# Kernel tuning notes

Measured on AMD Instinct MI355X. Metric: run time of the kernel, lower is better.

Reference implementation:

```python
import jax, jax.numpy as jnp
import numpy as np
from functools import partial

HID = 256
HOR = 5

def _lin(k, i, o):
    return jax.random.normal(k, (i, o), jnp.float32) / np.sqrt(i)

def setup_inputs() -> dict:
    key = jax.random.key(0)
    ks = jax.random.split(key, 32)
    B, T, D, Hf, Wf = 4, 16, 768, 16, 16
    H, W = 1024, 1024
    inp = {}
    inp['features'] = jax.random.normal(ks[0], (B, T, D, Hf, Wf), jnp.float32)
    inp['predictions'] = jax.random.uniform(ks[1], (B, T, 1, H, W), dtype=jnp.float32)
    # position encoder: 4 -> HID -> HID
    inp['pe_w1'] = _lin(ks[2], 4, HID); inp['pe_b1'] = jnp.zeros((HID,), jnp.float32)
    inp['pe_w2'] = _lin(ks[3], HID, HID); inp['pe_b2'] = jnp.zeros((HID,), jnp.float32)
    # 2-layer LSTM, gate order i,f,g,o (torch convention)
    inp['wih0'] = _lin(ks[4], HID, 4 * HID); inp['whh0'] = _lin(ks[5], HID, 4 * HID)
    inp['bih0'] = jnp.zeros((4 * HID,), jnp.float32); inp['bhh0'] = jnp.zeros((4 * HID,), jnp.float32)
    inp['wih1'] = _lin(ks[6], HID, 4 * HID); inp['whh1'] = _lin(ks[7], HID, 4 * HID)
    inp['bih1'] = jnp.zeros((4 * HID,), jnp.float32); inp['bhh1'] = jnp.zeros((4 * HID,), jnp.float32)
    # motion predictor: HID -> HID -> HID/2 -> HOR*4
    inp['mp_w1'] = _lin(ks[8], HID, HID); inp['mp_b1'] = jnp.zeros((HID,), jnp.float32)
    inp['mp_w2'] = _lin(ks[9], HID, HID // 2); inp['mp_b2'] = jnp.zeros((HID // 2,), jnp.float32)
    inp['mp_w3'] = _lin(ks[10], HID // 2, HOR * 4); inp['mp_b3'] = jnp.zeros((HOR * 4,), jnp.float32)
    # confidence: HID -> HID/2 -> HOR
    inp['cf_w1'] = _lin(ks[11], HID, HID // 2); inp['cf_b1'] = jnp.zeros((HID // 2,), jnp.float32)
    inp['cf_w2'] = _lin(ks[12], HID // 2, HOR); inp['cf_b2'] = jnp.zeros((HOR,), jnp.float32)
    return inp

def _extract_bboxes(predictions):
    # predictions: (B,T,1,H,W) -> bboxes (B,T,4) in (cx,cy,w,h), normalized
    B, T, _, H, W = predictions.shape
    mask = predictions[:, :, 0] > 0.5  # (B,T,H,W)
    xs = jnp.arange(W, dtype=jnp.float32)           # (W,)
    ys = jnp.arange(H, dtype=jnp.float32)[:, None]  # (H,1)
    big = jnp.float32(H + W)
    x_min = jnp.min(jnp.where(mask, xs, big), axis=(-2, -1))
    x_max = jnp.max(jnp.where(mask, xs, -1.0), axis=(-2, -1))
    y_min = jnp.min(jnp.where(mask, ys, big), axis=(-2, -1))
    y_max = jnp.max(jnp.where(mask, ys, -1.0), axis=(-2, -1))
    has = jnp.any(mask, axis=(-2, -1))  # (B,T)
    cx = (x_min + x_max) / 2.0 / W
    cy = (y_min + y_max) / 2.0 / H
    w = (x_max - x_min) / W
    h = (y_max - y_min) / H
    bbox = jnp.stack([cx, cy, w, h], axis=-1)  # (B,T,4)
    default = jnp.array([0.5, 0.5, 0.1, 0.1], dtype=jnp.float32)
    return jnp.where(has[..., None], bbox, default)

def _lstm_layer(x, wih, whh, bih, bhh):
    # x: (B,T,HID); returns (hs (B,T,H), h_final (B,H))
    B = x.shape[0]
    xg = jnp.einsum('bti,ig->btg', x, wih) + bih  # (B,T,4H)
    def step(carry, xg_t):
        h, c = carry
        g = xg_t + h @ whh + bhh
        i, f, gg, o = jnp.split(g, 4, axis=-1)
        i = jax.nn.sigmoid(i); f = jax.nn.sigmoid(f)
        gg = jnp.tanh(gg); o = jax.nn.sigmoid(o)
        c = f * c + i * gg
        h = o * jnp.tanh(c)
        return (h, c), h
    z = jnp.zeros((B, HID), x.dtype)
    (h, c), hs = jax.lax.scan(step, (z, z), xg.swapaxes(0, 1))
    return hs.swapaxes(0, 1), h

def reference(features, predictions, pe_w1, pe_b1, pe_w2, pe_b2,
              wih0, whh0, bih0, bhh0, wih1, whh1, bih1, bhh1,
              mp_w1, mp_b1, mp_w2, mp_b2, mp_w3, mp_b3,
              cf_w1, cf_b1, cf_w2, cf_b2):
    B, T = features.shape[:2]
    bboxes = _extract_bboxes(predictions)  # (B,T,4)
    pos = jax.nn.relu(bboxes @ pe_w1 + pe_b1)
    pos = jax.nn.relu(pos @ pe_w2 + pe_b2)  # (B,T,HID)
    h1, _ = _lstm_layer(pos, wih0, whh0, bih0, bhh0)
    motion_features, last_hidden = _lstm_layer(h1, wih1, whh1, bih1, bhh1)
    x = jax.nn.relu(last_hidden @ mp_w1 + mp_b1)
    x = jax.nn.relu(x @ mp_w2 + mp_b2)
    predicted_deltas = (x @ mp_w3 + mp_b3).reshape(B, HOR, 4)
    last_bbox = bboxes[:, -1:, :]
    predicted_bboxes = last_bbox + jnp.cumsum(predicted_deltas, axis=1)
    c = jax.nn.relu(last_hidden @ cf_w1 + cf_b1)
    confidence = jax.nn.sigmoid(c @ cf_w2 + cf_b2)  # (B,HOR)
    predicted_locations = predicted_bboxes[..., :2]
    predicted_scales = predicted_bboxes[..., 2:]
    return (predicted_deltas, predicted_bboxes, predicted_locations,
            predicted_scales, motion_features, confidence, bboxes)
```

## Files before the change

### kernel.cpp

```cpp
#include <hip/hip_runtime.h>
#include <math.h>

#define BIGI (1 << 30)

#define PM_OFF    0
#define HT0_OFF   8192
#define HT2_OFF   40960
#define DONE_OFF  45056
#define ZERO_BEG  8192
#define ZERO_END  45057

#define OUT_DELTAS 0
#define OUT_PBB    80
#define OUT_LOC    160
#define OUT_SCL    200
#define OUT_MF     240
#define OUT_CONF   16624
#define OUT_BBOX   16644

__device__ __forceinline__ float sigmoidf_(float x) { return 1.0f / (1.0f + expf(-x)); }

__device__ __forceinline__ void storeh(unsigned long long* p, float h, int tag) {
    unsigned long long v =
        ((unsigned long long)(unsigned)tag << 32) | (unsigned long long)__float_as_uint(h);
    __hip_atomic_store(p, v, __ATOMIC_RELAXED, __HIP_MEMORY_SCOPE_AGENT);
}
__device__ __forceinline__ float pollh(const unsigned long long* p, int tag) {
    unsigned long long v = __hip_atomic_load(p, __ATOMIC_RELAXED, __HIP_MEMORY_SCOPE_AGENT);
    while ((int)(v >> 32) != tag) {
        __builtin_amdgcn_s_sleep(1);
        v = __hip_atomic_load(p, __ATOMIC_RELAXED, __HIP_MEMORY_SCOPE_AGENT);
    }
    return __uint_as_float((unsigned)v);
}

__global__ __launch_bounds__(256) void k_minmax(const float4* __restrict__ pred,
                                                int* __restrict__ ws) {
    int tid = threadIdx.x;
    for (int i = ZERO_BEG + blockIdx.x * 256 + tid; i < ZERO_END; i += 2048 * 256)
        ws[i] = 0;
    int img = blockIdx.x >> 5;
    int chunk = blockIdx.x & 31;
    int base = img * 262144 + chunk * 8192 + tid;
    int xmn = BIGI, xmx = -1, ymn = BIGI, ymx = -1;
#pragma unroll 4
    for (int i = 0; i < 32; ++i) {
        int idx4 = base + i * 256;
        float4 v = pred[idx4];
        int x = (idx4 << 2) & 1023;
        int y = (idx4 >> 8) & 1023;
        bool m0 = v.x > 0.5f, m1 = v.y > 0.5f, m2 = v.z > 0.5f, m3 = v.w > 0.5f;
        int cmn = m0 ? x : (m1 ? x + 1 : (m2 ? x + 2 : (m3 ? x + 3 : BIGI)));
        int cmx = m3 ? x + 3 : (m2 ? x + 2 : (m1 ? x + 1 : (m0 ? x : -1)));
        xmn = min(xmn, cmn);
        xmx = max(xmx, cmx);
        if (m0 | m1 | m2 | m3) { ymn = min(ymn, y); ymx = max(ymx, y); }
    }
    for (int off = 32; off > 0; off >>= 1) {
        xmn = min(xmn, __shfl_down(xmn, off));
        xmx = max(xmx, __shfl_down(xmx, off));
        ymn = min(ymn, __shfl_down(ymn, off));
        ymx = max(ymx, __shfl_down(ymx, off));
    }
    __shared__ int red[4][4];
    int wave = tid >> 6;
    if ((tid & 63) == 0) { red[0][wave] = xmn; red[1][wave] = xmx; red[2][wave] = ymn; red[3][wave] = ymx; }
    __syncthreads();
    if (tid == 0) {
        xmn = min(min(red[0][0], red[0][1]), min(red[0][2], red[0][3]));
        xmx = max(max(red[1][0], red[1][1]), max(red[1][2], red[1][3]));
        ymn = min(min(red[2][0], red[2][1]), min(red[2][2], red[2][3]));
        ymx = max(max(red[3][0], red[3][1]), max(red[3][2], red[3][3]));
        ((int4*)(ws + PM_OFF))[blockIdx.x] = make_int4(xmn, xmx, ymn, ymx);
    }
}

__device__ __forceinline__ void mk_bbox(int xmn, int xmx, int ymn, int ymx,
                                        float* o) {
    if (xmx >= 0) {
        o[0] = (float)(xmn + xmx) * (0.5f / 1024.0f);
        o[1] = (float)(ymn + ymx) * (0.5f / 1024.0f);
        o[2] = (float)(xmx - xmn) * (1.0f / 1024.0f);
        o[3] = (float)(ymx - ymn) * (1.0f / 1024.0f);
    } else { o[0] = 0.5f; o[1] = 0.5f; o[2] = 0.1f; o[3] = 0.1f; }
}

__global__ __launch_bounds__(256, 1) void k_fused(
    const float* __restrict__ pe_w1, const float* __restrict__ pe_b1,
    const float* __restrict__ pe_w2, const float* __restrict__ pe_b2,
    const float* __restrict__ wih0, const float* __restrict__ whh0,
    const float* __restrict__ bih0, const float* __restrict__ bhh0,
    const float* __restrict__ wih1, const float* __restrict__ whh1,
    const float* __restrict__ bih1, const float* __restrict__ bhh1,
    const float* __restrict__ mp_w1, const float* __restrict__ mp_b1,
    const float* __restrict__ mp_w2, const float* __restrict__ mp_b2,
    const float* __restrict__ mp_w3, const float* __restrict__ mp_b3,
    const float* __restrict__ cf_w1, const float* __restrict__ cf_b1,
    const float* __restrict__ cf_w2, const float* __restrict__ cf_b2,
    const int4* __restrict__ pm4, unsigned long long* __restrict__ hT0,
    unsigned long long* __restrict__ hT2, int* __restrict__ done,
    float* __restrict__ out) {
    __shared__ float sPX[4096];
    __shared__ float sP1[4096];
    __shared__ float sBB[64];
    __shared__ float hsm[256];
    __shared__ float h2sm[256];
    __shared__ float part[256];
    const int tid = threadIdx.x, blk = blockIdx.x;

    if (blk >= 64) {
        float a0 = 0.f, a1 = 1.f, a2 = 2.f, a3 = 3.f, a4 = 4.f, a5 = 5.f, a6 = 6.f, a7 = 7.f;
        const float m = 1.0000001f, c = 0.9999999f;
        for (;;) {
#pragma unroll
            for (int i = 0; i < 128; ++i) {
                a0 = fmaf(a0, m, c); a1 = fmaf(a1, m, c); a2 = fmaf(a2, m, c); a3 = fmaf(a3, m, c);
                a4 = fmaf(a4, m, c); a5 = fmaf(a5, m, c); a6 = fmaf(a6, m, c); a7 = fmaf(a7, m, c);
            }
            if (__hip_atomic_load(done, __ATOMIC_RELAXED, __HIP_MEMORY_SCOPE_AGENT) >= 4) break;
        }
        asm volatile("" :: "v"(a0), "v"(a1), "v"(a2), "v"(a3), "v"(a4), "v"(a5), "v"(a6), "v"(a7));
        return;
    }

    const int layer = blk >> 5;
    const int b = (blk >> 3) & 3, g = blk & 7;
    const int j = tid & 127, kh = tid >> 7;
    const int col = ((j >> 5) << 8) + g * 32 + (j & 31);

    if (layer == 0) {
        {
            int il = tid >> 4, c2 = (tid & 15) * 2;
            int4 A = pm4[(b * 16 + il) * 32 + c2];
            int4 B = pm4[(b * 16 + il) * 32 + c2 + 1];
            int xmn = min(A.x, B.x), xmx = max(A.y, B.y);
            int ymn = min(A.z, B.z), ymx = max(A.w, B.w);
            for (int off = 8; off > 0; off >>= 1) {
                xmn = min(xmn, __shfl_down(xmn, off, 16));
                xmx = max(xmx, __shfl_down(xmx, off, 16));
                ymn = min(ymn, __shfl_down(ymn, off, 16));
                ymx = max(ymx, __shfl_down(ymx, off, 16));
            }
            if ((tid & 15) == 0) {
                float bb[4];
                mk_bbox(xmn, xmx, ymn, ymx, bb);
                sBB[il * 4 + 0] = bb[0]; sBB[il * 4 + 1] = bb[1];
                sBB[il * 4 + 2] = bb[2]; sBB[il * 4 + 3] = bb[3];
                if (g == 0) {
                    out[OUT_BBOX + (b * 16 + il) * 4 + 0] = bb[0];
                    out[OUT_BBOX + (b * 16 + il) * 4 + 1] = bb[1];
                    out[OUT_BBOX + (b * 16 + il) * 4 + 2] = bb[2];
                    out[OUT_BBOX + (b * 16 + il) * 4 + 3] = bb[3];
                }
            }
        }
        __syncthreads();
        {
            float w0 = pe_w1[tid], w1 = pe_w1[256 + tid];
            float w2 = pe_w1[512 + tid], w3 = pe_w1[768 + tid], b1v = pe_b1[tid];
#pragma unroll
            for (int i = 0; i < 16; ++i) {
                float v = sBB[i * 4] * w0 + sBB[i * 4 + 1] * w1 +
                          sBB[i * 4 + 2] * w2 + sBB[i * 4 + 3] * w3 + b1v;
                sP1[i * 256 + tid] = fmaxf(v, 0.0f);
            }
        }
        __syncthreads();
        {
            float acc[16];
            float b2v = pe_b2[tid];
#pragma unroll
            for (int i = 0; i < 16; ++i) acc[i] = b2v;
            for (int k = 0; k < 256; ++k) {
                float wv = pe_w2[k * 256 + tid];
#pragma unroll
                for (int i = 0; i < 16; ++i) acc[i] += sP1[i * 256 + k] * wv;
            }
#pragma unroll
            for (int i = 0; i < 16; ++i) sPX[i * 256 + tid] = fmaxf(acc[i], 0.0f);
        }
        __syncthreads();
    }

    const float* wih = layer ? wih1 : wih0;
    const float* whh = layer ? whh1 : whh0;
    const float* bih = layer ? bih1 : bih0;
    const float* bhh = layer ? bhh1 : bhh0;
    float4 wi[32], wh[32];
#pragma unroll
    for (int k4 = 0; k4 < 32; ++k4) {
        int r = kh * 128 + k4 * 4;
        wi[k4].x = wih[(r + 0) * 1024 + col];
        wi[k4].y = wih[(r + 1) * 1024 + col];
        wi[k4].z = wih[(r + 2) * 1024 + col];
        wi[k4].w = wih[(r + 3) * 1024 + col];
        wh[k4].x = whh[(r + 0) * 1024 + col];
        wh[k4].y = whh[(r + 1) * 1024 + col];
        wh[k4].z = whh[(r + 2) * 1024 + col];
        wh[k4].w = whh[(r + 3) * 1024 + col];
    }
    float bs0 = 0.f, bs1 = 0.f, bs2 = 0.f, bs3 = 0.f;
    if (tid < 32) {
        int u = g * 32 + tid;
        bs0 = bih[u] + bhh[u];
        bs1 = bih[256 + u] + bhh[256 + u];
        bs2 = bih[512 + u] + bhh[512 + u];
        bs3 = bih[768 + u] + bhh[768 + u];
    }

    float cst = 0.0f;
    for (int t = 0; t < 16; ++t) {
        if (layer == 0) {
            if (t) hsm[tid] = pollh(&hT0[((b * 16 + t - 1) << 8) + tid], t);
        } else {
            hsm[tid] = pollh(&hT0[((b * 16 + t) << 8) + tid], t + 1);
            if (t) h2sm[tid] = pollh(&hT2[(((b << 1) | ((t - 1) & 1)) << 8) + tid], t);
        }
        __syncthreads();
        float a = 0.0f;
        if (layer == 0) {
            const float4* xr = (const float4*)&sPX[t * 256 + kh * 128];
#pragma unroll
            for (int k = 0; k < 32; ++k) {
                float4 x = xr[k];
                a += x.x * wi[k].x + x.y * wi[k].y + x.z * wi[k].z + x.w * wi[k].w;
            }
            if (t) {
                const float4* hr = (const float4*)&hsm[kh * 128];
#pragma unroll
                for (int k = 0; k < 32; ++k) {
                    float4 h = hr[k];
                    a += h.x * wh[k].x + h.y * wh[k].y + h.z * wh[k].z + h.w * wh[k].w;
                }
            }
        } else {
            const float4* xr = (const float4*)&hsm[kh * 128];
#pragma unroll
            for (int k = 0; k < 32; ++k) {
                float4 x = xr[k];
                a += x.x * wi[k].x + x.y * wi[k].y + x.z * wi[k].z + x.w * wi[k].w;
            }
            if (t) {
                const float4* hr = (const float4*)&h2sm[kh * 128];
#pragma unroll
                for (int k = 0; k < 32; ++k) {
                    float4 h = hr[k];
                    a += h.x * wh[k].x + h.y * wh[k].y + h.z * wh[k].z + h.w * wh[k].w;
                }
            }
        }
        part[tid] = a;
        __syncthreads();
        if (tid < 32) {
            float gi = part[tid] + part[128 + tid] + bs0;
            float gf = part[32 + tid] + part[160 + tid] + bs1;
            float gg = part[64 + tid] + part[192 + tid] + bs2;
            float go = part[96 + tid] + part[224 + tid] + bs3;
            float i_ = sigmoidf_(gi), f_ = sigmoidf_(gf);
            float g_ = tanhf(gg), o_ = sigmoidf_(go);
            cst = f_ * cst + i_ * g_;
            float h = o_ * tanhf(cst);
            int unit = g * 32 + tid;
            if (layer == 0) {
                storeh(&hT0[((b * 16 + t) << 8) + unit], h, t + 1);
            } else {
                storeh(&hT2[(((b << 1) | (t & 1)) << 8) + unit], h, t + 1);
                out[OUT_MF + (b * 16 + t) * 256 + unit] = h;
            }
        }
    }
    if (layer == 0 || g != 0) return;

    float* lh = sPX;
    float* x1 = sPX + 256;
    float* c1 = sPX + 512;
    float* x2 = sPX + 640;
    float* dl = sPX + 768;
    lh[tid] = pollh(&hT2[(((b << 1) | 1) << 8) + tid], 16);
    if (tid < 32) {
        int4 v = pm4[(b * 16 + 15) * 32 + tid];
        int xmn = v.x, xmx = v.y, ymn = v.z, ymx = v.w;
        for (int off = 16; off > 0; off >>= 1) {
            xmn = min(xmn, __shfl_down(xmn, off, 32));
            xmx = max(xmx, __shfl_down(xmx, off, 32));
            ymn = min(ymn, __shfl_down(ymn, off, 32));
            ymx = max(ymx, __shfl_down(ymx, off, 32));
        }
        if (tid == 0) mk_bbox(xmn, xmx, ymn, ymx, sBB);
    }
    __syncthreads();
    {
        float a = mp_b1[tid];
#pragma unroll 4
        for (int k = 0; k < 256; ++k) a += lh[k] * mp_w1[k * 256 + tid];
        x1[tid] = fmaxf(a, 0.0f);
    }
    if (tid < 128) {
        float a = cf_b1[tid];
#pragma unroll 4
        for (int k = 0; k < 256; ++k) a += lh[k] * cf_w1[k * 128 + tid];
        c1[tid] = fmaxf(a, 0.0f);
    }
    __syncthreads();
    if (tid < 128) {
        float a = mp_b2[tid];
#pragma unroll 4
        for (int k = 0; k < 256; ++k) a += x1[k] * mp_w2[k * 128 + tid];
        x2[tid] = fmaxf(a, 0.0f);
    } else if (tid < 133) {
        int jj = tid - 128;
        float a = cf_b2[jj];
#pragma unroll 4
        for (int k = 0; k < 128; ++k) a += c1[k] * cf_w2[k * 5 + jj];
        out[OUT_CONF + b * 5 + jj] = sigmoidf_(a);
    }
    __syncthreads();
    if (tid < 20) {
        float a = mp_b3[tid];
#pragma unroll 4
        for (int k = 0; k < 128; ++k) a += x2[k] * mp_w3[k * 20 + tid];
        dl[tid] = a;
        out[OUT_DELTAS + b * 20 + tid] = a;
    }
    __syncthreads();
    if (tid < 4) {
        float acc = sBB[tid];
        for (int hh = 0; hh < 5; ++hh) {
            acc += dl[hh * 4 + tid];
            out[OUT_PBB + b * 20 + hh * 4 + tid] = acc;
            if (tid < 2) out[OUT_LOC + b * 10 + hh * 2 + tid] = acc;
            else out[OUT_SCL + b * 10 + hh * 2 + (tid - 2)] = acc;
        }
    }
    __syncthreads();
    if (tid == 0) atomicAdd(done, 1);
}

extern "C" void kernel_launch(void* const* d_in, const int* in_sizes, int n_in,
                              void* d_out, int out_size, void* d_ws, size_t ws_size,
                              hipStream_t stream) {
    (void)in_sizes; (void)n_in; (void)out_size; (void)ws_size;
    const float* pred = (const float*)d_in[1];
    const float* pe_w1 = (const float*)d_in[2];
    const float* pe_b1 = (const float*)d_in[3];
    const float* pe_w2 = (const float*)d_in[4];
    const float* pe_b2 = (const float*)d_in[5];
    const float* wih0 = (const float*)d_in[6];
    const float* whh0 = (const float*)d_in[7];
    const float* bih0 = (const float*)d_in[8];
    const float* bhh0 = (const float*)d_in[9];
    const float* wih1 = (const float*)d_in[10];
    const float* whh1 = (const float*)d_in[11];
    const float* bih1 = (const float*)d_in[12];
    const float* bhh1 = (const float*)d_in[13];
    const float* mp_w1 = (const float*)d_in[14];
    const float* mp_b1 = (const float*)d_in[15];
    const float* mp_w2 = (const float*)d_in[16];
    const float* mp_b2 = (const float*)d_in[17];
    const float* mp_w3 = (const float*)d_in[18];
    const float* mp_b3 = (const float*)d_in[19];
    const float* cf_w1 = (const float*)d_in[20];
    const float* cf_b1 = (const float*)d_in[21];
    const float* cf_w2 = (const float*)d_in[22];
    const float* cf_b2 = (const float*)d_in[23];
    float* out = (float*)d_out;
    int* wsi = (int*)d_ws;

    hipLaunchKernelGGL(k_minmax, dim3(64 * 32), dim3(256), 0, stream,
                       (const float4*)pred, wsi);
    hipLaunchKernelGGL(k_fused, dim3(192), dim3(256), 0, stream,
                       pe_w1, pe_b1, pe_w2, pe_b2,
                       wih0, whh0, bih0, bhh0,
                       wih1, whh1, bih1, bhh1,
                       mp_w1, mp_b1, mp_w2, mp_b2, mp_w3, mp_b3,
                       cf_w1, cf_b1, cf_w2, cf_b2,
                       (const int4*)(wsi + PM_OFF),
                       (unsigned long long*)(wsi + HT0_OFF),
                       (unsigned long long*)(wsi + HT2_OFF),
                       wsi + DONE_OFF, out);
}
```

Before: 603.6 us.

## Split LSTM recurrence across 16 unit groups and precompute layer-0 input gates

Doubles the per-batch LSTM workers from 8 to 16 blocks per layer (16 units each, 4-way K split), so each thread keeps half as many weight registers. Layer 0 precomputes its input-projection gates for all timesteps before the recurrence, so the serial loop only does the hidden-state matvec. Layer 1 polls both dependency slots in one combined helper, and the spinning filler blocks are adjusted for the new grid of 256. The cost is a wider cross-block polling fan-in per step and extra shared memory.

```diff
diff --git a/kernel.cpp b/kernel.cpp
--- a/kernel.cpp
+++ b/kernel.cpp
@@ -32,6 +32,20 @@
         v = __hip_atomic_load(p, __ATOMIC_RELAXED, __HIP_MEMORY_SCOPE_AGENT);
     }
     return __uint_as_float((unsigned)v);
+}
+__device__ __forceinline__ float2 pollh2(const unsigned long long* p1, int tag1,
+                                         const unsigned long long* p2, int tag2) {
+    unsigned long long v1 = __hip_atomic_load(p1, __ATOMIC_RELAXED, __HIP_MEMORY_SCOPE_AGENT);
+    unsigned long long v2 = __hip_atomic_load(p2, __ATOMIC_RELAXED, __HIP_MEMORY_SCOPE_AGENT);
+    while ((int)(v1 >> 32) != tag1) {
+        __builtin_amdgcn_s_sleep(1);
+        v1 = __hip_atomic_load(p1, __ATOMIC_RELAXED, __HIP_MEMORY_SCOPE_AGENT);
+    }
+    while ((int)(v2 >> 32) != tag2) {
+        __builtin_amdgcn_s_sleep(1);
+        v2 = __hip_atomic_load(p2, __ATOMIC_RELAXED, __HIP_MEMORY_SCOPE_AGENT);
+    }
+    return make_float2(__uint_as_float((unsigned)v1), __uint_as_float((unsigned)v2));
 }
 
 __global__ __launch_bounds__(256) void k_minmax(const float4* __restrict__ pred,
@@ -75,8 +89,7 @@
     }
 }
 
-__device__ __forceinline__ void mk_bbox(int xmn, int xmx, int ymn, int ymx,
-                                        float* o) {
+__device__ __forceinline__ void mk_bbox(int xmn, int xmx, int ymn, int ymx, float* o) {
     if (xmx >= 0) {
         o[0] = (float)(xmn + xmx) * (0.5f / 1024.0f);
         o[1] = (float)(ymn + ymx) * (0.5f / 1024.0f);
@@ -100,20 +113,21 @@
     const int4* __restrict__ pm4, unsigned long long* __restrict__ hT0,
     unsigned long long* __restrict__ hT2, int* __restrict__ done,
     float* __restrict__ out) {
-    __shared__ float sPX[4096];
-    __shared__ float sP1[4096];
+    __shared__ __align__(16) float sPX[4096];
+    __shared__ __align__(16) float sP1[4096];
+    __shared__ float xgl[1024];
+    __shared__ __align__(16) float hsm[256];
+    __shared__ __align__(16) float h2sm[256];
+    __shared__ float partA[256];
     __shared__ float sBB[64];
-    __shared__ float hsm[256];
-    __shared__ float h2sm[256];
-    __shared__ float part[256];
     const int tid = threadIdx.x, blk = blockIdx.x;
 
-    if (blk >= 64) {
+    if (blk >= 128) {
         float a0 = 0.f, a1 = 1.f, a2 = 2.f, a3 = 3.f, a4 = 4.f, a5 = 5.f, a6 = 6.f, a7 = 7.f;
         const float m = 1.0000001f, c = 0.9999999f;
         for (;;) {
-#pragma unroll
-            for (int i = 0; i < 128; ++i) {
+#pragma unroll 8
+            for (int i = 0; i < 512; ++i) {
                 a0 = fmaf(a0, m, c); a1 = fmaf(a1, m, c); a2 = fmaf(a2, m, c); a3 = fmaf(a3, m, c);
                 a4 = fmaf(a4, m, c); a5 = fmaf(a5, m, c); a6 = fmaf(a6, m, c); a7 = fmaf(a7, m, c);
             }
@@ -123,10 +137,27 @@
         return;
     }
 
-    const int layer = blk >> 5;
-    const int b = (blk >> 3) & 3, g = blk & 7;
-    const int j = tid & 127, kh = tid >> 7;
-    const int col = ((j >> 5) << 8) + g * 32 + (j & 31);
+    const int layer = blk >> 6;
+    const int b = (blk >> 4) & 3, g = blk & 15;
+    const int cidx = tid & 63, kq = tid >> 6;
+    const int gate = cidx >> 4, u = cidx & 15;
+    const int col = gate * 256 + g * 16 + u;
+    const int krow0 = kq * 64;
+
+    const float* wih = layer ? wih1 : wih0;
+    const float* whh = layer ? whh1 : whh0;
+    const float* bih = layer ? bih1 : bih0;
+    const float* bhh = layer ? bhh1 : bhh0;
+
+    float4 wvi[16];
+#pragma unroll
+    for (int k4 = 0; k4 < 16; ++k4) {
+        int r = krow0 + k4 * 4;
+        wvi[k4].x = wih[(r + 0) * 1024 + col];
+        wvi[k4].y = wih[(r + 1) * 1024 + col];
+        wvi[k4].z = wih[(r + 2) * 1024 + col];
+        wvi[k4].w = wih[(r + 3) * 1024 + col];
+    }
 
     if (layer == 0) {
         {
@@ -180,32 +211,44 @@
             for (int i = 0; i < 16; ++i) sPX[i * 256 + tid] = fmaxf(acc[i], 0.0f);
         }
         __syncthreads();
-    }
-
-    const float* wih = layer ? wih1 : wih0;
-    const float* whh = layer ? whh1 : whh0;
-    const float* bih = layer ? bih1 : bih0;
-    const float* bhh = layer ? bhh1 : bhh0;
-    float4 wi[32], wh[32];
-#pragma unroll
-    for (int k4 = 0; k4 < 32; ++k4) {
-        int r = kh * 128 + k4 * 4;
-        wi[k4].x = wih[(r + 0) * 1024 + col];
-        wi[k4].y = wih[(r + 1) * 1024 + col];
-        wi[k4].z = wih[(r + 2) * 1024 + col];
-        wi[k4].w = wih[(r + 3) * 1024 + col];
-        wh[k4].x = whh[(r + 0) * 1024 + col];
-        wh[k4].y = whh[(r + 1) * 1024 + col];
-        wh[k4].z = whh[(r + 2) * 1024 + col];
-        wh[k4].w = whh[(r + 3) * 1024 + col];
+        float bsum = 0.0f;
+        if (tid < 64) {
+            int cc = (tid >> 4) * 256 + g * 16 + (tid & 15);
+            bsum = bih[cc] + bhh[cc];
+        }
+        for (int t = 0; t < 16; ++t) {
+            const float4* xr = (const float4*)&sPX[t * 256 + krow0];
+            float a = 0.0f;
+#pragma unroll
+            for (int k = 0; k < 16; ++k) {
+                float4 x = xr[k];
+                a += x.x * wvi[k].x + x.y * wvi[k].y + x.z * wvi[k].z + x.w * wvi[k].w;
+            }
+            partA[tid] = a;
+            __syncthreads();
+            if (tid < 64)
+                xgl[t * 64 + tid] = partA[tid] + partA[64 + tid] +
+                                    partA[128 + tid] + partA[192 + tid] + bsum;
+            __syncthreads();
+        }
+    }
+
+    float4 wvh[16];
+#pragma unroll
+    for (int k4 = 0; k4 < 16; ++k4) {
+        int r = krow0 + k4 * 4;
+        wvh[k4].x = whh[(r + 0) * 1024 + col];
+        wvh[k4].y = whh[(r + 1) * 1024 + col];
+        wvh[k4].z = whh[(r + 2) * 1024 + col];
+        wvh[k4].w = whh[(r + 3) * 1024 + col];
     }
     float bs0 = 0.f, bs1 = 0.f, bs2 = 0.f, bs3 = 0.f;
-    if (tid < 32) {
-        int u = g * 32 + tid;
-        bs0 = bih[u] + bhh[u];
-        bs1 = bih[256 + u] + bhh[256 + u];
-        bs2 = bih[512 + u] + bhh[512 + u];
-        bs3 = bih[768 + u] + bhh[768 + u];
+    if (layer == 1 && tid < 16) {
+        int uu = g * 16 + tid;
+        bs0 = bih[uu] + bhh[uu];
+        bs1 = bih[256 + uu] + bhh[256 + uu];
+        bs2 = bih[512 + uu] + bhh[512 + uu];
+        bs3 = bih[768 + uu] + bhh[768 + uu];
     }
 
     float cst = 0.0f;
@@ -213,54 +256,61 @@
         if (layer == 0) {
             if (t) hsm[tid] = pollh(&hT0[((b * 16 + t - 1) << 8) + tid], t);
         } else {
-            hsm[tid] = pollh(&hT0[((b * 16 + t) << 8) + tid], t + 1);
-            if (t) h2sm[tid] = pollh(&hT2[(((b << 1) | ((t - 1) & 1)) << 8) + tid], t);
+            if (t) {
+                float2 hv = pollh2(&hT0[((b * 16 + t) << 8) + tid], t + 1,
+                                   &hT2[(((b << 1) | ((t - 1) & 1)) << 8) + tid], t);
+                hsm[tid] = hv.x; h2sm[tid] = hv.y;
+            } else {
+                hsm[tid] = pollh(&hT0[((b * 16) << 8) + tid], 1);
+            }
         }
         __syncthreads();
         float a = 0.0f;
         if (layer == 0) {
-            const float4* xr = (const float4*)&sPX[t * 256 + kh * 128];
-#pragma unroll
-            for (int k = 0; k < 32; ++k) {
+            if (t) {
+                const float4* hr = (const float4*)&hsm[krow0];
+#pragma unroll
+                for (int k = 0; k < 16; ++k) {
+                    float4 h = hr[k];
+                    a += h.x * wvh[k].x + h.y * wvh[k].y + h.z * wvh[k].z + h.w * wvh[k].w;
+                }
+            }
+        } else {
+            const float4* xr = (const float4*)&hsm[krow0];
+#pragma unroll
+            for (int k = 0; k < 16; ++k) {
                 float4 x = xr[k];
-                a += x.x * wi[k].x + x.y * wi[k].y + x.z * wi[k].z + x.w * wi[k].w;
+                a += x.x * wvi[k].x + x.y * wvi[k].y + x.z * wvi[k].z + x.w * wvi[k].w;
             }
             if (t) {
-                const float4* hr = (const float4*)&hsm[kh * 128];
-#pragma unroll
-                for (int k = 0; k < 32; ++k) {
+                const float4* hr = (const float4*)&h2sm[krow0];
+#pragma unroll
+                for (int k = 0; k < 16; ++k) {
                     float4 h = hr[k];
-                    a += h.x * wh[k].x + h.y * wh[k].y + h.z * wh[k].z + h.w * wh[k].w;
+                    a += h.x * wvh[k].x + h.y * wvh[k].y + h.z * wvh[k].z + h.w * wvh[k].w;
                 }
             }
-        } else {
-            const float4* xr = (const float4*)&hsm[kh * 128];
-#pragma unroll
-            for (int k = 0; k < 32; ++k) {
-                float4 x = xr[k];
-                a += x.x * wi[k].x + x.y * wi[k].y + x.z * wi[k].z + x.w * wi[k].w;
-            }
-            if (t) {
-                const float4* hr = (const float4*)&h2sm[kh * 128];
-#pragma unroll
-                for (int k = 0; k < 32; ++k) {
-                    float4 h = hr[k];
-                    a += h.x * wh[k].x + h.y * wh[k].y + h.z * wh[k].z + h.w * wh[k].w;
-                }
-            }
-        }
-        part[tid] = a;
+        }
+        partA[tid] = a;
         __syncthreads();
-        if (tid < 32) {
-            float gi = part[tid] + part[128 + tid] + bs0;
-            float gf = part[32 + tid] + part[160 + tid] + bs1;
-            float gg = part[64 + tid] + part[192 + tid] + bs2;
-            float go = part[96 + tid] + part[224 + tid] + bs3;
+        if (tid < 16) {
+            float gi, gf, gg, go;
+            if (layer == 0) {
+                gi = xgl[t * 64 + tid];       gf = xgl[t * 64 + 16 + tid];
+                gg = xgl[t * 64 + 32 + tid];  go = xgl[t * 64 + 48 + tid];
+            } else { gi = bs0; gf = bs1; gg = bs2; go = bs3; }
+#pragma unroll
+            for (int q = 0; q < 4; ++q) {
+                gi += partA[q * 64 + tid];
+                gf += partA[q * 64 + 16 + tid];
+                gg += partA[q * 64 + 32 + tid];
+                go += partA[q * 64 + 48 + tid];
+            }
             float i_ = sigmoidf_(gi), f_ = sigmoidf_(gf);
             float g_ = tanhf(gg), o_ = sigmoidf_(go);
             cst = f_ * cst + i_ * g_;
             float h = o_ * tanhf(cst);
-            int unit = g * 32 + tid;
+            int unit = g * 16 + tid;
             if (layer == 0) {
                 storeh(&hT0[((b * 16 + t) << 8) + unit], h, t + 1);
             } else {
@@ -368,7 +418,7 @@
 
     hipLaunchKernelGGL(k_minmax, dim3(64 * 32), dim3(256), 0, stream,
                        (const float4*)pred, wsi);
-    hipLaunchKernelGGL(k_fused, dim3(192), dim3(256), 0, stream,
+    hipLaunchKernelGGL(k_fused, dim3(256), dim3(256), 0, stream,
                        pe_w1, pe_b1, pe_w2, pe_b2,
                        wih0, whh0, bih0, bhh0,
                        wih1, whh1, bih1, bhh1,
```

After: 594.4 us. Within noise of the previous version (-1.5%).

## Restructure LSTM into three pipelined stages with precomputed input projections

Applied to the files above, without the earlier changes.

Splits the fused LSTM kernel into three block stages. Stage 0 precomputes the layer-0 input projection for all timesteps and then runs the layer-0 recurrence. Stage 1 computes the layer-1 input projection per timestep and publishes it through a tagged workspace buffer. Stage 2 runs only the layer-1 recurrence. Blocks grow to 512 threads with 64 units each, and the dummy spin blocks that kept clocks up are removed, so each recurrent step carries only one matvec on its critical path. In exchange it adds a cross-block handoff, zeroes a larger workspace, and raises register pressure at two blocks per CU.

```diff
diff --git a/kernel.cpp b/kernel.cpp
--- a/kernel.cpp
+++ b/kernel.cpp
@@ -6,9 +6,9 @@
 #define PM_OFF    0
 #define HT0_OFF   8192
 #define HT2_OFF   40960
-#define DONE_OFF  45056
+#define XG1_OFF   45056
 #define ZERO_BEG  8192
-#define ZERO_END  45057
+#define ZERO_END  176128
 
 #define OUT_DELTAS 0
 #define OUT_PBB    80
@@ -37,8 +37,10 @@
 __global__ __launch_bounds__(256) void k_minmax(const float4* __restrict__ pred,
                                                 int* __restrict__ ws) {
     int tid = threadIdx.x;
-    for (int i = ZERO_BEG + blockIdx.x * 256 + tid; i < ZERO_END; i += 2048 * 256)
-        ws[i] = 0;
+    {
+        int i = ZERO_BEG + blockIdx.x * 256 + tid;
+        if (i < ZERO_END) ws[i] = 0;
+    }
     int img = blockIdx.x >> 5;
     int chunk = blockIdx.x & 31;
     int base = img * 262144 + chunk * 8192 + tid;
@@ -75,8 +77,7 @@
     }
 }
 
-__device__ __forceinline__ void mk_bbox(int xmn, int xmx, int ymn, int ymx,
-                                        float* o) {
+__device__ __forceinline__ void mk_bbox(int xmn, int xmx, int ymn, int ymx, float* o) {
     if (xmx >= 0) {
         o[0] = (float)(xmn + xmx) * (0.5f / 1024.0f);
         o[1] = (float)(ymn + ymx) * (0.5f / 1024.0f);
@@ -85,7 +86,7 @@
     } else { o[0] = 0.5f; o[1] = 0.5f; o[2] = 0.1f; o[3] = 0.1f; }
 }
 
-__global__ __launch_bounds__(256, 1) void k_fused(
+__global__ __launch_bounds__(512, 2) void k_fused(
     const float* __restrict__ pe_w1, const float* __restrict__ pe_b1,
     const float* __restrict__ pe_w2, const float* __restrict__ pe_b2,
     const float* __restrict__ wih0, const float* __restrict__ whh0,
@@ -98,50 +99,36 @@
     const float* __restrict__ cf_w1, const float* __restrict__ cf_b1,
     const float* __restrict__ cf_w2, const float* __restrict__ cf_b2,
     const int4* __restrict__ pm4, unsigned long long* __restrict__ hT0,
-    unsigned long long* __restrict__ hT2, int* __restrict__ done,
+    unsigned long long* __restrict__ hT2, unsigned long long* __restrict__ xg1,
     float* __restrict__ out) {
-    __shared__ float sPX[4096];
-    __shared__ float sP1[4096];
+    __shared__ __align__(16) float sA[4096];
+    __shared__ __align__(16) float sB[4096];
+    __shared__ __align__(16) float hsm[256];
+    __shared__ float xsm[256];
+    __shared__ float partA[512];
     __shared__ float sBB[64];
-    __shared__ float hsm[256];
-    __shared__ float h2sm[256];
-    __shared__ float part[256];
     const int tid = threadIdx.x, blk = blockIdx.x;
-
-    if (blk >= 64) {
-        float a0 = 0.f, a1 = 1.f, a2 = 2.f, a3 = 3.f, a4 = 4.f, a5 = 5.f, a6 = 6.f, a7 = 7.f;
-        const float m = 1.0000001f, c = 0.9999999f;
-        for (;;) {
-#pragma unroll
-            for (int i = 0; i < 128; ++i) {
-                a0 = fmaf(a0, m, c); a1 = fmaf(a1, m, c); a2 = fmaf(a2, m, c); a3 = fmaf(a3, m, c);
-                a4 = fmaf(a4, m, c); a5 = fmaf(a5, m, c); a6 = fmaf(a6, m, c); a7 = fmaf(a7, m, c);
-            }
-            if (__hip_atomic_load(done, __ATOMIC_RELAXED, __HIP_MEMORY_SCOPE_AGENT) >= 4) break;
-        }
-        asm volatile("" :: "v"(a0), "v"(a1), "v"(a2), "v"(a3), "v"(a4), "v"(a5), "v"(a6), "v"(a7));
-        return;
-    }
-
-    const int layer = blk >> 5;
-    const int b = (blk >> 3) & 3, g = blk & 7;
-    const int j = tid & 127, kh = tid >> 7;
-    const int col = ((j >> 5) << 8) + g * 32 + (j & 31);
-
-    if (layer == 0) {
+    const int stage = blk >> 4;
+    const int b = (blk >> 2) & 3, g = blk & 3;
+    const int c = tid & 255, kh = tid >> 8;
+    const int col = ((c >> 6) << 8) + g * 64 + (c & 63);
+    const int krow0 = kh * 128;
+
+    float4 wreg[32];
+    float cst = 0.0f;
+
+    if (stage == 0) {
         {
-            int il = tid >> 4, c2 = (tid & 15) * 2;
-            int4 A = pm4[(b * 16 + il) * 32 + c2];
-            int4 B = pm4[(b * 16 + il) * 32 + c2 + 1];
-            int xmn = min(A.x, B.x), xmx = max(A.y, B.y);
-            int ymn = min(A.z, B.z), ymx = max(A.w, B.w);
-            for (int off = 8; off > 0; off >>= 1) {
-                xmn = min(xmn, __shfl_down(xmn, off, 16));
-                xmx = max(xmx, __shfl_down(xmx, off, 16));
-                ymn = min(ymn, __shfl_down(ymn, off, 16));
-                ymx = max(ymx, __shfl_down(ymx, off, 16));
-            }
-            if ((tid & 15) == 0) {
+            int il = tid >> 5, ch = tid & 31;
+            int4 v = pm4[(b * 16 + il) * 32 + ch];
+            int xmn = v.x, xmx = v.y, ymn = v.z, ymx = v.w;
+            for (int off = 16; off > 0; off >>= 1) {
+                xmn = min(xmn, __shfl_down(xmn, off, 32));
+                xmx = max(xmx, __shfl_down(xmx, off, 32));
+                ymn = min(ymn, __shfl_down(ymn, off, 32));
+                ymx = max(ymx, __shfl_down(ymx, off, 32));
+            }
+            if (ch == 0) {
                 float bb[4];
                 mk_bbox(xmn, xmx, ymn, ymx, bb);
                 sBB[il * 4 + 0] = bb[0]; sBB[il * 4 + 1] = bb[1];
@@ -155,128 +142,182 @@
             }
         }
         __syncthreads();
-        {
+        if (tid < 256) {
             float w0 = pe_w1[tid], w1 = pe_w1[256 + tid];
             float w2 = pe_w1[512 + tid], w3 = pe_w1[768 + tid], b1v = pe_b1[tid];
 #pragma unroll
             for (int i = 0; i < 16; ++i) {
                 float v = sBB[i * 4] * w0 + sBB[i * 4 + 1] * w1 +
                           sBB[i * 4 + 2] * w2 + sBB[i * 4 + 3] * w3 + b1v;
-                sP1[i * 256 + tid] = fmaxf(v, 0.0f);
+                sB[i * 256 + tid] = fmaxf(v, 0.0f);
             }
         }
         __syncthreads();
         {
-            float acc[16];
-            float b2v = pe_b2[tid];
-#pragma unroll
-            for (int i = 0; i < 16; ++i) acc[i] = b2v;
+            int i0 = kh * 8;
+            float acc[8];
+            float b2v = pe_b2[c];
+#pragma unroll
+            for (int i = 0; i < 8; ++i) acc[i] = b2v;
             for (int k = 0; k < 256; ++k) {
-                float wv = pe_w2[k * 256 + tid];
-#pragma unroll
-                for (int i = 0; i < 16; ++i) acc[i] += sP1[i * 256 + k] * wv;
-            }
-#pragma unroll
-            for (int i = 0; i < 16; ++i) sPX[i * 256 + tid] = fmaxf(acc[i], 0.0f);
-        }
-        __syncthreads();
-    }
-
-    const float* wih = layer ? wih1 : wih0;
-    const float* whh = layer ? whh1 : whh0;
-    const float* bih = layer ? bih1 : bih0;
-    const float* bhh = layer ? bhh1 : bhh0;
-    float4 wi[32], wh[32];
-#pragma unroll
-    for (int k4 = 0; k4 < 32; ++k4) {
-        int r = kh * 128 + k4 * 4;
-        wi[k4].x = wih[(r + 0) * 1024 + col];
-        wi[k4].y = wih[(r + 1) * 1024 + col];
-        wi[k4].z = wih[(r + 2) * 1024 + col];
-        wi[k4].w = wih[(r + 3) * 1024 + col];
-        wh[k4].x = whh[(r + 0) * 1024 + col];
-        wh[k4].y = whh[(r + 1) * 1024 + col];
-        wh[k4].z = whh[(r + 2) * 1024 + col];
-        wh[k4].w = whh[(r + 3) * 1024 + col];
-    }
-    float bs0 = 0.f, bs1 = 0.f, bs2 = 0.f, bs3 = 0.f;
-    if (tid < 32) {
-        int u = g * 32 + tid;
-        bs0 = bih[u] + bhh[u];
-        bs1 = bih[256 + u] + bhh[256 + u];
-        bs2 = bih[512 + u] + bhh[512 + u];
-        bs3 = bih[768 + u] + bhh[768 + u];
-    }
-
-    float cst = 0.0f;
-    for (int t = 0; t < 16; ++t) {
-        if (layer == 0) {
-            if (t) hsm[tid] = pollh(&hT0[((b * 16 + t - 1) << 8) + tid], t);
-        } else {
-            hsm[tid] = pollh(&hT0[((b * 16 + t) << 8) + tid], t + 1);
-            if (t) h2sm[tid] = pollh(&hT2[(((b << 1) | ((t - 1) & 1)) << 8) + tid], t);
-        }
-        __syncthreads();
-        float a = 0.0f;
-        if (layer == 0) {
-            const float4* xr = (const float4*)&sPX[t * 256 + kh * 128];
+                float wv = pe_w2[k * 256 + c];
+#pragma unroll
+                for (int i = 0; i < 8; ++i) acc[i] += sB[(i0 + i) * 256 + k] * wv;
+            }
+#pragma unroll
+            for (int i = 0; i < 8; ++i) sA[(i0 + i) * 256 + c] = fmaxf(acc[i], 0.0f);
+        }
+        __syncthreads();
+#pragma unroll
+        for (int k4 = 0; k4 < 32; ++k4) {
+            int r = krow0 + k4 * 4;
+            wreg[k4].x = wih0[(r + 0) * 1024 + col];
+            wreg[k4].y = wih0[(r + 1) * 1024 + col];
+            wreg[k4].z = wih0[(r + 2) * 1024 + col];
+            wreg[k4].w = wih0[(r + 3) * 1024 + col];
+        }
+        float xacc[16];
+#pragma unroll
+        for (int t = 0; t < 16; ++t) {
+            const float4* pr = (const float4*)&sA[t * 256 + krow0];
+            float a = 0.0f;
 #pragma unroll
             for (int k = 0; k < 32; ++k) {
-                float4 x = xr[k];
-                a += x.x * wi[k].x + x.y * wi[k].y + x.z * wi[k].z + x.w * wi[k].w;
-            }
+                float4 x = pr[k];
+                a += x.x * wreg[k].x + x.y * wreg[k].y + x.z * wreg[k].z + x.w * wreg[k].w;
+            }
+            xacc[t] = a;
+        }
+        if (kh == 1) {
+#pragma unroll
+            for (int t = 0; t < 16; ++t) sB[t * 256 + c] = xacc[t];
+        }
+        __syncthreads();
+        if (kh == 0) {
+            float bsum = bih0[col] + bhh0[col];
+#pragma unroll
+            for (int t = 0; t < 16; ++t) sB[t * 256 + c] = xacc[t] + sB[t * 256 + c] + bsum;
+        }
+        __syncthreads();
+#pragma unroll
+        for (int k4 = 0; k4 < 32; ++k4) {
+            int r = krow0 + k4 * 4;
+            wreg[k4].x = whh0[(r + 0) * 1024 + col];
+            wreg[k4].y = whh0[(r + 1) * 1024 + col];
+            wreg[k4].z = whh0[(r + 2) * 1024 + col];
+            wreg[k4].w = whh0[(r + 3) * 1024 + col];
+        }
+        for (int t = 0; t < 16; ++t) {
+            if (t && tid < 256) hsm[tid] = pollh(&hT0[((b * 16 + t - 1) << 8) + tid], t);
+            __syncthreads();
+            float a = 0.0f;
             if (t) {
-                const float4* hr = (const float4*)&hsm[kh * 128];
+                const float4* hr = (const float4*)&hsm[krow0];
 #pragma unroll
                 for (int k = 0; k < 32; ++k) {
                     float4 h = hr[k];
-                    a += h.x * wh[k].x + h.y * wh[k].y + h.z * wh[k].z + h.w * wh[k].w;
+                    a += h.x * wreg[k].x + h.y * wreg[k].y + h.z * wreg[k].z + h.w * wreg[k].w;
                 }
             }
+            partA[kh * 256 + c] = a;
+            __syncthreads();
+            if (tid < 64) {
+                int u = tid, unit = g * 64 + u;
+                float gi = sB[t * 256 + u]       + partA[u]       + partA[256 + u];
+                float gf = sB[t * 256 + 64 + u]  + partA[64 + u]  + partA[320 + u];
+                float gg = sB[t * 256 + 128 + u] + partA[128 + u] + partA[384 + u];
+                float go = sB[t * 256 + 192 + u] + partA[192 + u] + partA[448 + u];
+                float i_ = sigmoidf_(gi), f_ = sigmoidf_(gf);
+                float g_ = tanhf(gg), o_ = sigmoidf_(go);
+                cst = f_ * cst + i_ * g_;
+                float h = o_ * tanhf(cst);
+                storeh(&hT0[((b * 16 + t) << 8) + unit], h, t + 1);
+            }
+        }
+        return;
+    }
+
+    if (stage == 1) {
+#pragma unroll
+        for (int k4 = 0; k4 < 32; ++k4) {
+            int r = krow0 + k4 * 4;
+            wreg[k4].x = wih1[(r + 0) * 1024 + col];
+            wreg[k4].y = wih1[(r + 1) * 1024 + col];
+            wreg[k4].z = wih1[(r + 2) * 1024 + col];
+            wreg[k4].w = wih1[(r + 3) * 1024 + col];
+        }
+        float bsum = 0.0f;
+        if (tid < 256) bsum = bih1[col] + bhh1[col];
+        for (int t = 0; t < 16; ++t) {
+            if (tid < 256) hsm[tid] = pollh(&hT0[((b * 16 + t) << 8) + tid], t + 1);
+            __syncthreads();
+            const float4* hr = (const float4*)&hsm[krow0];
+            float a = 0.0f;
+#pragma unroll
+            for (int k = 0; k < 32; ++k) {
+                float4 h = hr[k];
+                a += h.x * wreg[k].x + h.y * wreg[k].y + h.z * wreg[k].z + h.w * wreg[k].w;
+            }
+            partA[kh * 256 + c] = a;
+            __syncthreads();
+            if (tid < 256) {
+                float v = partA[tid] + partA[256 + tid] + bsum;
+                storeh(&xg1[((b * 16 + t) << 10) + col], v, t + 1);
+            }
+        }
+        return;
+    }
+
+#pragma unroll
+    for (int k4 = 0; k4 < 32; ++k4) {
+        int r = krow0 + k4 * 4;
+        wreg[k4].x = whh1[(r + 0) * 1024 + col];
+        wreg[k4].y = whh1[(r + 1) * 1024 + col];
+        wreg[k4].z = whh1[(r + 2) * 1024 + col];
+        wreg[k4].w = whh1[(r + 3) * 1024 + col];
+    }
+    for (int t = 0; t < 16; ++t) {
+        if (tid < 256) {
+            if (t) hsm[tid] = pollh(&hT2[(((b << 1) | ((t - 1) & 1)) << 8) + tid], t);
         } else {
-            const float4* xr = (const float4*)&hsm[kh * 128];
+            int cc = tid - 256;
+            int colx = ((cc >> 6) << 8) + g * 64 + (cc & 63);
+            xsm[cc] = pollh(&xg1[((b * 16 + t) << 10) + colx], t + 1);
+        }
+        __syncthreads();
+        float a = 0.0f;
+        if (t) {
+            const float4* hr = (const float4*)&hsm[krow0];
 #pragma unroll
             for (int k = 0; k < 32; ++k) {
-                float4 x = xr[k];
-                a += x.x * wi[k].x + x.y * wi[k].y + x.z * wi[k].z + x.w * wi[k].w;
-            }
-            if (t) {
-                const float4* hr = (const float4*)&h2sm[kh * 128];
-#pragma unroll
-                for (int k = 0; k < 32; ++k) {
-                    float4 h = hr[k];
-                    a += h.x * wh[k].x + h.y * wh[k].y + h.z * wh[k].z + h.w * wh[k].w;
-                }
-            }
-        }
-        part[tid] = a;
-        __syncthreads();
-        if (tid < 32) {
-            float gi = part[tid] + part[128 + tid] + bs0;
-            float gf = part[32 + tid] + part[160 + tid] + bs1;
-            float gg = part[64 + tid] + part[192 + tid] + bs2;
-            float go = part[96 + tid] + part[224 + tid] + bs3;
+                float4 h = hr[k];
+                a += h.x * wreg[k].x + h.y * wreg[k].y + h.z * wreg[k].z + h.w * wreg[k].w;
+            }
+        }
+        partA[kh * 256 + c] = a;
+        __syncthreads();
+        if (tid < 64) {
+            int u = tid, unit = g * 64 + u;
+            float gi = xsm[u]       + partA[u]       + partA[256 + u];
+            float gf = xsm[64 + u]  + partA[64 + u]  + partA[320 + u];
+            float gg = xsm[128 + u] + partA[128 + u] + partA[384 + u];
+            float go = xsm[192 + u] + partA[192 + u] + partA[448 + u];
             float i_ = sigmoidf_(gi), f_ = sigmoidf_(gf);
             float g_ = tanhf(gg), o_ = sigmoidf_(go);
             cst = f_ * cst + i_ * g_;
             float h = o_ * tanhf(cst);
-            int unit = g * 32 + tid;
-            if (layer == 0) {
-                storeh(&hT0[((b * 16 + t) << 8) + unit], h, t + 1);
-            } else {
-                storeh(&hT2[(((b << 1) | (t & 1)) << 8) + unit], h, t + 1);
-                out[OUT_MF + (b * 16 + t) * 256 + unit] = h;
-            }
-        }
-    }
-    if (layer == 0 || g != 0) return;
-
-    float* lh = sPX;
-    float* x1 = sPX + 256;
-    float* c1 = sPX + 512;
-    float* x2 = sPX + 640;
-    float* dl = sPX + 768;
-    lh[tid] = pollh(&hT2[(((b << 1) | 1) << 8) + tid], 16);
+            storeh(&hT2[(((b << 1) | (t & 1)) << 8) + unit], h, t + 1);
+            out[OUT_MF + (b * 16 + t) * 256 + unit] = h;
+        }
+    }
+    if (g != 0) return;
+
+    float* lh = sA;
+    float* x1 = sA + 256;
+    float* c1 = sA + 512;
+    float* x2 = sA + 640;
+    float* dl = sA + 768;
+    if (tid < 256) lh[tid] = pollh(&hT2[(((b << 1) | 1) << 8) + tid], 16);
     if (tid < 32) {
         int4 v = pm4[(b * 16 + 15) * 32 + tid];
         int xmn = v.x, xmx = v.y, ymn = v.z, ymx = v.w;
@@ -289,17 +330,17 @@
         if (tid == 0) mk_bbox(xmn, xmx, ymn, ymx, sBB);
     }
     __syncthreads();
-    {
+    if (tid < 256) {
         float a = mp_b1[tid];
 #pragma unroll 4
         for (int k = 0; k < 256; ++k) a += lh[k] * mp_w1[k * 256 + tid];
         x1[tid] = fmaxf(a, 0.0f);
-    }
-    if (tid < 128) {
-        float a = cf_b1[tid];
-#pragma unroll 4
-        for (int k = 0; k < 256; ++k) a += lh[k] * cf_w1[k * 128 + tid];
-        c1[tid] = fmaxf(a, 0.0f);
+    } else if (tid < 384) {
+        int jj = tid - 256;
+        float a = cf_b1[jj];
+#pragma unroll 4
+        for (int k = 0; k < 256; ++k) a += lh[k] * cf_w1[k * 128 + jj];
+        c1[jj] = fmaxf(a, 0.0f);
     }
     __syncthreads();
     if (tid < 128) {
@@ -307,8 +348,8 @@
 #pragma unroll 4
         for (int k = 0; k < 256; ++k) a += x1[k] * mp_w2[k * 128 + tid];
         x2[tid] = fmaxf(a, 0.0f);
-    } else if (tid < 133) {
-        int jj = tid - 128;
+    } else if (tid >= 256 && tid < 261) {
+        int jj = tid - 256;
         float a = cf_b2[jj];
 #pragma unroll 4
         for (int k = 0; k < 128; ++k) a += c1[k] * cf_w2[k * 5 + jj];
@@ -332,8 +373,6 @@
             else out[OUT_SCL + b * 10 + hh * 2 + (tid - 2)] = acc;
         }
     }
-    __syncthreads();
-    if (tid == 0) atomicAdd(done, 1);
 }
 
 extern "C" void kernel_launch(void* const* d_in, const int* in_sizes, int n_in,
@@ -368,7 +407,7 @@
 
     hipLaunchKernelGGL(k_minmax, dim3(64 * 32), dim3(256), 0, stream,
                        (const float4*)pred, wsi);
-    hipLaunchKernelGGL(k_fused, dim3(192), dim3(256), 0, stream,
+    hipLaunchKernelGGL(k_fused, dim3(48), dim3(512), 0, stream,
                        pe_w1, pe_b1, pe_w2, pe_b2,
                        wih0, whh0, bih0, bhh0,
                        wih1, whh1, bih1, bhh1,
@@ -377,5 +416,6 @@
                        (const int4*)(wsi + PM_OFF),
                        (unsigned long long*)(wsi + HT0_OFF),
                        (unsigned long long*)(wsi + HT2_OFF),
-                       wsi + DONE_OFF, out);
-}
+                       (unsigned long long*)(wsi + XG1_OFF),
+                       out);
+}
```

Result: faster. 559.5 us (median of 2 runs) (-7.3%).
